# Kernel tuning notes

Measured on AMD Instinct MI355X. Metric: run time of the kernel, lower is better.

## Reference

```python
import jax, jax.numpy as jnp
import numpy as np

B, T, V, H = 1, 1024, 32000, 2048
NH, NKV, HD = 8, 4, 256
QS, KVS = NH * HD, NKV * HD
I, L = 8192, 2
SCALE = 256.0 ** -0.5          # query_pre_attn_scalar ** -0.5
ATTN_CAP, FINAL_CAP = 50.0, 30.0
WIN, EPS, THETA = 512, 1e-6, 10000.0
NEG = -2.3819763e38


def setup_inputs() -> dict:
    key = jax.random.key(0)
    ks = jax.random.split(key, 12)
    s = 0.02
    return {
        "tokens": jax.random.randint(ks[0], (B, T), 0, V, dtype=jnp.int32),
        "embed": jax.random.normal(ks[1], (V, H), jnp.float32) * s,
        "qkv_w": jax.random.normal(ks[2], (L, (NH + 2 * NKV) * HD, H), jnp.float32) * s,
        "o_w": jax.random.normal(ks[3], (L, H, NH * HD), jnp.float32) * s,
        "gate_w": jax.random.normal(ks[4], (L, I, H), jnp.float32) * s,
        "up_w": jax.random.normal(ks[5], (L, I, H), jnp.float32) * s,
        "down_w": jax.random.normal(ks[6], (L, H, I), jnp.float32) * s,
        "ln_in": jax.random.normal(ks[7], (L, H), jnp.float32) * s,   # RMSNorm weight (zeros-init offset)
        "ln_pa": jax.random.normal(ks[8], (L, H), jnp.float32) * s,
        "ln_pre": jax.random.normal(ks[9], (L, H), jnp.float32) * s,
        "ln_post": jax.random.normal(ks[10], (L, H), jnp.float32) * s,
        "ln_f": jax.random.normal(ks[11], (H,), jnp.float32) * s,
    }


def rmsnorm(x, w):
    x = x.astype(jnp.float32)
    n = x * jax.lax.rsqrt(jnp.mean(x * x, axis=-1, keepdims=True) + EPS)
    return n * (1.0 + w)  # add_unit_offset=True


def rope(x, cos, sin):
    # x: [B, T, N, HD]; split-half complex rotary as in apply_rotary_emb
    x1, x2 = jnp.split(x, 2, axis=-1)
    c = cos[None, :, None, :]
    s = sin[None, :, None, :]
    return jnp.concatenate([x1 * c - x2 * s, x1 * s + x2 * c], axis=-1)


def reference(tokens, embed, qkv_w, o_w, gate_w, up_w, down_w,
              ln_in, ln_pa, ln_pre, ln_post, ln_f):
    pos = jnp.arange(T)
    inv = 1.0 / (THETA ** (jnp.arange(0, HD, 2, dtype=jnp.float32) / HD))  # [HD/2]
    ang = pos.astype(jnp.float32)[:, None] * inv[None, :]
    cos, sin = jnp.cos(ang), jnp.sin(ang)

    i, j = pos[:, None], pos[None, :]
    causal = j <= i
    mask_global = jnp.where(causal, 0.0, NEG).astype(jnp.float32)
    mask_local = jnp.where(causal & (i - j < WIN), 0.0, NEG).astype(jnp.float32)
    masks = [mask_local, mask_global]  # layer 0: LOCAL_SLIDING, layer 1: GLOBAL

    x = embed[tokens] * jnp.sqrt(jnp.float32(H))  # Gemma embedding normalizer

    for l in range(L):
        h = rmsnorm(x, ln_in[l])
        qkv = jnp.einsum('bth,oh->bto', h, qkv_w[l])
        q = qkv[..., :QS].reshape(B, T, NH, HD)
        k = qkv[..., QS:QS + KVS].reshape(B, T, NKV, HD)
        v = qkv[..., QS + KVS:].reshape(B, T, NKV, HD)
        q = rope(q, cos, sin)
        k = rope(k, cos, sin)
        # prefill: kv_write_indices=arange(T) -> cache == current k/v
        k = jnp.repeat(k, NH // NKV, axis=2)  # GQA repeat_interleave over heads
        v = jnp.repeat(v, NH // NKV, axis=2)
        scores = jnp.einsum('bqhd,bkhd->bhqk', q * SCALE, k)
        scores = jnp.tanh(scores / ATTN_CAP) * ATTN_CAP
        scores = scores + masks[l][None, None]
        attn = jax.nn.softmax(scores.astype(jnp.float32), axis=-1)
        out = jnp.einsum('bhqk,bkhd->bqhd', attn, v).reshape(B, T, NH * HD)
        out = jnp.einsum('bto,ho->bth', out, o_w[l])
        x = x + rmsnorm(out, ln_pa[l])

        h = rmsnorm(x, ln_pre[l])
        gate = jax.nn.gelu(jnp.einsum('bth,ih->bti', h, gate_w[l]), approximate=True)
        up = jnp.einsum('bth,ih->bti', h, up_w[l])
        ff = jnp.einsum('bti,hi->bth', gate * up, down_w[l])
        x = x + rmsnorm(ff, ln_post[l])

    x = rmsnorm(x, ln_f)
    logits = jnp.einsum('bth,vh->btv', x, embed)
    logits = jnp.tanh(logits / FINAL_CAP) * FINAL_CAP  # final_logit_softcapping
    return logits
```

## Files before the change

### kernel.cpp

```cpp
#include <hip/hip_runtime.h>
#include <hip/hip_bf16.h>
#include <math.h>

typedef unsigned short u16;
typedef __attribute__((ext_vector_type(8))) short bf16x8;
typedef __attribute__((ext_vector_type(4))) float f32x4;
typedef __attribute__((ext_vector_type(4))) u16 u16x4;

#define T_SEQ 1024
#define HDIM  2048
#define NHEAD 8
#define NKVH  4
#define HSZ   256
#define ISZ   8192
#define NVOC  32000

#define GLDS(src, dst) __builtin_amdgcn_global_load_lds( \
    (const __attribute__((address_space(1))) void*)(src), \
    (__attribute__((address_space(3))) void*)(dst), 16, 0, 0)

__device__ __forceinline__ u16 f2bf(float f) {
    union { float f; unsigned u; } v; v.f = f;
    return (u16)((v.u + 0x7fffu + ((v.u >> 16) & 1u)) >> 16);
}
__device__ __forceinline__ float bf2f(u16 h) {
    union { unsigned u; float f; } v; v.u = (unsigned)h << 16; return v.f;
}

__device__ __forceinline__ float fast_tanh(float x) {
    float e = __expf(-2.0f * fabsf(x));
    float t = (1.0f - e) / (1.0f + e);
    return copysignf(t, x);
}

__device__ __forceinline__ f32x4 mfma16(bf16x8 a, bf16x8 b, f32x4 c) {
    return __builtin_amdgcn_mfma_f32_16x16x32_bf16(a, b, c, 0, 0, 0);
}

__global__ __launch_bounds__(256)
void cvt_bf16(const float* __restrict__ s, u16* __restrict__ d, long n4)
{
    for (long i = blockIdx.x * 256L + threadIdx.x; i < n4; i += (long)gridDim.x * 256) {
        f32x4 v = ((const f32x4*)s)[i];
        u16x4 o;
        o.x = f2bf(v.x); o.y = f2bf(v.y); o.z = f2bf(v.z); o.w = f2bf(v.w);
        ((u16x4*)d)[i] = o;
    }
}

template<int EPI>
__global__ __launch_bounds__(512, 1)
void gemm_dp(const u16* __restrict__ A, int lda,
             const u16* __restrict__ B, int ldb,
             float* __restrict__ C, int ldc, long sC, int K)
{
    extern __shared__ u16 lds[];
    const int t = threadIdx.x;
    const int lane = t & 63, wid = t >> 6;
    const int z = blockIdx.z;
    A += (long)z * K;
    B += (long)z * K;
    C += (long)z * sC;

    const int nwg = gridDim.x * gridDim.y;
    int flat = blockIdx.y * gridDim.x + blockIdx.x;
    {
        const int q = nwg >> 3, r = nwg & 7;
        const int xcd = flat & 7, loc = flat >> 3;
        flat = (xcd < r ? xcd * (q + 1) : r * (q + 1) + (xcd - r) * q) + loc;
    }
    const int gm = gridDim.y;
    const long m0 = (long)(flat % gm) * 128;
    const long n0 = (long)(flat / gm) * 256;

    const int sr = t >> 3;
    const int sl = ((t & 7) ^ (sr & 7)) * 8;
    const u16* gA0 = A + (m0 + sr)       * (long)lda + sl;
    const u16* gA1 = A + (m0 + 64 + sr)  * (long)lda + sl;
    const u16* gB0 = B + (n0 + sr)       * (long)ldb + sl;
    const u16* gB1 = B + (n0 + 64 + sr)  * (long)ldb + sl;
    const u16* gB2 = B + (n0 + 128 + sr) * (long)ldb + sl;
    const u16* gB3 = B + (n0 + 192 + sr) * (long)ldb + sl;

    auto stage = [&](int kt) {
        const long ko = (long)kt * 64;
        char* d = (char*)lds + (kt % 3) * 49152 + t * 16;
        GLDS(gA0 + ko, d);
        GLDS(gA1 + ko, d + 8192);
        GLDS(gB0 + ko, d + 16384);
        GLDS(gB1 + ko, d + 24576);
        GLDS(gB2 + ko, d + 32768);
        GLDS(gB3 + ko, d + 40960);
    };

    f32x4 acc[4][4] = {};
    const int fr = lane & 15, kq = lane >> 4;
    const int wm = wid >> 2, wn = wid & 3;
    const int ps0 = ((kq)     ^ (lane & 7)) * 8;
    const int ps1 = ((4 + kq) ^ (lane & 7)) * 8;

    const int KT = K >> 6;
    stage(0);
    if (KT > 1) stage(1);
    if (KT > 2) stage(2);

    for (int kt = 0; kt < KT; ++kt) {
        if (kt < KT - 2)       asm volatile("s_waitcnt vmcnt(12)" ::: "memory");
        else if (kt == KT - 2) asm volatile("s_waitcnt vmcnt(6)" ::: "memory");
        else                   asm volatile("s_waitcnt vmcnt(0)" ::: "memory");
        __builtin_amdgcn_s_barrier();

        const u16* Asl = lds + (kt % 3) * 24576;
        const u16* Bsl = Asl + 8192;
        #pragma unroll
        for (int kk = 0; kk < 2; ++kk) {
            const int ps = kk ? ps1 : ps0;
            bf16x8 af[4], bfv[4];
            #pragma unroll
            for (int mi = 0; mi < 4; ++mi)
                af[mi] = *(const bf16x8*)(Asl + (wm * 64 + mi * 16 + fr) * 64 + ps);
            #pragma unroll
            for (int ni = 0; ni < 4; ++ni)
                bfv[ni] = *(const bf16x8*)(Bsl + (wn * 64 + ni * 16 + fr) * 64 + ps);
            #pragma unroll
            for (int mi = 0; mi < 4; ++mi)
                #pragma unroll
                for (int ni = 0; ni < 4; ++ni)
                    acc[mi][ni] = mfma16(af[mi], bfv[ni], acc[mi][ni]);
        }
        __builtin_amdgcn_s_barrier();
        if (kt + 3 < KT) stage(kt + 3);
    }

    const int crb = kq * 4, ccol = fr;
    #pragma unroll
    for (int mi = 0; mi < 4; ++mi) {
        #pragma unroll
        for (int rr = 0; rr < 4; ++rr) {
            const long row = m0 + wm * 64 + mi * 16 + crb + rr;
            float* cp = C + row * ldc + n0 + wn * 64 + ccol;
            #pragma unroll
            for (int ni = 0; ni < 4; ++ni) {
                float v = acc[mi][ni][rr];
                if (EPI == 1) v = fast_tanh(v * (1.0f / 30.0f)) * 30.0f;
                cp[ni * 16] = v;
            }
        }
    }
}

template<int EPI>
__global__ __launch_bounds__(512, 1)
void gemm8(const u16* __restrict__ A, int lda,
           const u16* __restrict__ B, int ldb,
           float* __restrict__ C, int ldc, long sC, int K)
{
    extern __shared__ u16 lds[];
    const int t = threadIdx.x;
    const int lane = t & 63, wid = t >> 6;
    const int z = blockIdx.z;
    A += (long)z * K;
    B += (long)z * K;
    C += (long)z * sC;

    const int nwg = gridDim.x * gridDim.y;
    int flat = blockIdx.y * gridDim.x + blockIdx.x;
    {
        const int q = nwg >> 3, r = nwg & 7;
        const int xcd = flat & 7, loc = flat >> 3;
        flat = (xcd < r ? xcd * (q + 1) : r * (q + 1) + (xcd - r) * q) + loc;
    }
    const int gm = gridDim.y;
    const long m0 = (long)(flat % gm) * 256;
    const long n0 = (long)(flat / gm) * 256;

    const int sr = t >> 3;
    const int sl = ((t & 7) ^ (sr & 7)) * 8;
    const u16* gA = A + (m0 + sr) * (long)lda + sl;
    const u16* gB = B + (n0 + sr) * (long)ldb + sl;

    auto stA = [&](int kt, int ro) {
        char* d = (char*)lds + (kt & 1) * 65536 + ro * 128 + t * 16;
        GLDS(gA + (long)ro * lda + (long)kt * 64, d);
    };
    auto stB = [&](int kt, int ro) {
        char* d = (char*)lds + (kt & 1) * 65536 + 32768 + ro * 128 + t * 16;
        GLDS(gB + (long)ro * ldb + (long)kt * 64, d);
    };

    f32x4 acc[8][4] = {};
    const int fr = lane & 15, kq = lane >> 4;
    const int wm = wid >> 2, wn = wid & 3;
    const int g0 = ((kq) ^ (lane & 7)) * 8;
    const int g1 = ((4 + kq) ^ (lane & 7)) * 8;
    const int KT = K >> 6;

    stA(0, 0); stA(0, 64); stA(0, 128); stA(0, 192);
    stB(0, 0); stB(0, 64); stB(0, 128); stB(0, 192);
    stA(1, 0); stA(1, 64); stA(1, 128); stA(1, 192);
    stB(1, 0); stB(1, 64); stB(1, 128); stB(1, 192);
    asm volatile("s_waitcnt vmcnt(8)" ::: "memory");
    __builtin_amdgcn_s_barrier();

    for (int kt = 0; kt < KT; ++kt) {
        const u16* As = lds + (kt & 1) * 32768;
        const u16* Bs = As + 16384;
        const int arow = wm * 128 + fr;
        const int brow = wn * 64 + fr;
        bf16x8 aL[4][2], aH[4][2], bL[2][2], bH[2][2];

        #pragma unroll
        for (int mi = 0; mi < 4; ++mi) {
            aL[mi][0] = *(const bf16x8*)(As + (arow + mi * 16) * 64 + g0);
            aL[mi][1] = *(const bf16x8*)(As + (arow + mi * 16) * 64 + g1);
        }
        #pragma unroll
        for (int ni = 0; ni < 2; ++ni) {
            bL[ni][0] = *(const bf16x8*)(Bs + (brow + ni * 16) * 64 + g0);
            bL[ni][1] = *(const bf16x8*)(Bs + (brow + ni * 16) * 64 + g1);
        }
        __builtin_amdgcn_s_setprio(1);
        #pragma unroll
        for (int mi = 0; mi < 4; ++mi)
            #pragma unroll
            for (int ni = 0; ni < 2; ++ni) {
                acc[mi][ni] = mfma16(aL[mi][0], bL[ni][0], acc[mi][ni]);
                acc[mi][ni] = mfma16(aL[mi][1], bL[ni][1], acc[mi][ni]);
            }
        __builtin_amdgcn_s_setprio(0);

        #pragma unroll
        for (int ni = 0; ni < 2; ++ni) {
            bH[ni][0] = *(const bf16x8*)(Bs + (brow + (ni + 2) * 16) * 64 + g0);
            bH[ni][1] = *(const bf16x8*)(Bs + (brow + (ni + 2) * 16) * 64 + g1);
        }
        __builtin_amdgcn_s_setprio(1);
        #pragma unroll
        for (int mi = 0; mi < 4; ++mi)
            #pragma unroll
            for (int ni = 0; ni < 2; ++ni) {
                acc[mi][ni + 2] = mfma16(aL[mi][0], bH[ni][0], acc[mi][ni + 2]);
                acc[mi][ni + 2] = mfma16(aL[mi][1], bH[ni][1], acc[mi][ni + 2]);
            }
        __builtin_amdgcn_s_setprio(0);
        __builtin_amdgcn_s_barrier();

        if (kt + 2 < KT) { stB(kt + 2, 0); stB(kt + 2, 64); stB(kt + 2, 128); stB(kt + 2, 192); }
        #pragma unroll
        for (int mi = 0; mi < 4; ++mi) {
            aH[mi][0] = *(const bf16x8*)(As + (arow + (mi + 4) * 16) * 64 + g0);
            aH[mi][1] = *(const bf16x8*)(As + (arow + (mi + 4) * 16) * 64 + g1);
        }
        __builtin_amdgcn_s_setprio(1);
        #pragma unroll
        for (int mi = 0; mi < 4; ++mi)
            #pragma unroll
            for (int ni = 0; ni < 2; ++ni) {
                acc[mi + 4][ni] = mfma16(aH[mi][0], bL[ni][0], acc[mi + 4][ni]);
                acc[mi + 4][ni] = mfma16(aH[mi][1], bL[ni][1], acc[mi + 4][ni]);
            }
        __builtin_amdgcn_s_setprio(0);
        __builtin_amdgcn_s_barrier();

        if (kt + 2 < KT) { stA(kt + 2, 0); stA(kt + 2, 64); stA(kt + 2, 128); stA(kt + 2, 192); }
        __builtin_amdgcn_s_setprio(1);
        #pragma unroll
        for (int mi = 0; mi < 4; ++mi)
            #pragma unroll
            for (int ni = 0; ni < 2; ++ni) {
                acc[mi + 4][ni + 2] = mfma16(aH[mi][0], bH[ni][0], acc[mi + 4][ni + 2]);
                acc[mi + 4][ni + 2] = mfma16(aH[mi][1], bH[ni][1], acc[mi + 4][ni + 2]);
            }
        __builtin_amdgcn_s_setprio(0);
        if (kt + 1 < KT) {
            if (kt + 2 < KT) asm volatile("s_waitcnt vmcnt(8)" ::: "memory");
            else             asm volatile("s_waitcnt vmcnt(0)" ::: "memory");
            __builtin_amdgcn_s_barrier();
        }
    }

    const int crb = kq * 4, ccol = fr;
    #pragma unroll
    for (int mj = 0; mj < 8; ++mj) {
        #pragma unroll
        for (int rr = 0; rr < 4; ++rr) {
            const long row = m0 + wm * 128 + mj * 16 + crb + rr;
            float* cp = C + row * ldc + n0 + wn * 64 + ccol;
            #pragma unroll
            for (int ni = 0; ni < 4; ++ni) {
                float v = acc[mj][ni][rr];
                if (EPI == 1) v = fast_tanh(v * (1.0f / 30.0f)) * 30.0f;
                cp[ni * 16] = v;
            }
        }
    }
}

template<int EPI, typename CT>
__global__ __launch_bounds__(256)
void gemm_bt(const u16* __restrict__ A, int lda, long sA,
             const u16* __restrict__ B, int ldb, long sB, int bshift,
             CT* __restrict__ C, int ldc, long sC, int K,
             int swin, int tflag)
{
    __shared__ u16 As[128 * 32];
    __shared__ u16 Bs[128 * 32];
    const int tid = threadIdx.x;
    const int lane = tid & 63, wid = tid >> 6;
    const int z = blockIdx.z;
    A += (long)z * sA;
    B += (long)(z >> bshift) * sB;
    C += (long)z * sC;

    const int nwg = gridDim.x * gridDim.y;
    int flat = blockIdx.y * gridDim.x + blockIdx.x;
    {
        const int q = nwg >> 3, r = nwg & 7;
        const int xcd = flat & 7, loc = flat >> 3;
        flat = (xcd < r ? xcd * (q + 1) : r * (q + 1) + (xcd - r) * q) + loc;
    }
    const int gm = gridDim.y;
    const long m0 = (long)(flat % gm) * 128;
    const long n0 = (long)(flat / gm) * 128;

    if (swin > 0) {
        if (n0 > m0 + 127) return;
        if (m0 - (n0 + 127) >= swin) return;
    }
    int klo = 0, khi = K;
    if (tflag > 0) {
        const long hi = m0 + 128;
        if (hi < khi) khi = (int)hi;
        const long lo = m0 - (long)tflag + 1;
        klo = lo > 0 ? (int)(lo & ~31L) : 0;
    }

    f32x4 acc[4][4] = {};

    const int ar = tid >> 2, ac = (tid & 3) * 8;
    const u16* gA0 = A + (m0 + ar) * lda + ac;
    const u16* gB0 = B + (n0 + ar) * (long)ldb + ac;
    const long a64 = 64L * lda, b64 = 64L * ldb;

    const int fr = lane & 15, fk = (lane >> 4) * 8;
    const int wm = (wid >> 1) * 64, wn = (wid & 1) * 64;

    for (int k0 = klo; k0 < khi; k0 += 32) {
        GLDS(gA0 + k0,       &As[tid * 8]);
        GLDS(gA0 + a64 + k0, &As[2048 + tid * 8]);
        GLDS(gB0 + k0,       &Bs[tid * 8]);
        GLDS(gB0 + b64 + k0, &Bs[2048 + tid * 8]);
        __syncthreads();
        bf16x8 af[4], bfv[4];
        #pragma unroll
        for (int mi = 0; mi < 4; ++mi)
            af[mi] = *(const bf16x8*)(&As[(wm + mi * 16 + fr) * 32 + fk]);
        #pragma unroll
        for (int ni = 0; ni < 4; ++ni)
            bfv[ni] = *(const bf16x8*)(&Bs[(wn + ni * 16 + fr) * 32 + fk]);
        #pragma unroll
        for (int mi = 0; mi < 4; ++mi)
            #pragma unroll
            for (int ni = 0; ni < 4; ++ni)
                acc[mi][ni] = mfma16(af[mi], bfv[ni], acc[mi][ni]);
        __syncthreads();
    }

    const int crb = (lane >> 4) * 4, ccol = lane & 15;
    #pragma unroll
    for (int mi = 0; mi < 4; ++mi) {
        #pragma unroll
        for (int rr = 0; rr < 4; ++rr) {
            const long row = m0 + wm + mi * 16 + crb + rr;
            CT* cp = C + row * ldc + n0 + wn + ccol;
            #pragma unroll
            for (int ni = 0; ni < 4; ++ni) {
                float v = acc[mi][ni][rr];
                if (EPI == 1) v = fast_tanh(v * (1.0f / 30.0f)) * 30.0f;
                if constexpr (sizeof(CT) == 2) cp[ni * 16] = f2bf(v);
                else                           cp[ni * 16] = v;
            }
        }
    }
}

__global__ __launch_bounds__(256)
void embed_scale(const int* __restrict__ tok, const float* __restrict__ emb,
                 float* __restrict__ x)
{
    const int t = blockIdx.x, tid = threadIdx.x;
    const long src = (long)tok[t] * HDIM;
    f32x4 a = *(const f32x4*)(emb + src + tid * 8);
    f32x4 b = *(const f32x4*)(emb + src + tid * 8 + 4);
    a *= 45.254834f; b *= 45.254834f;
    *(f32x4*)(x + (long)t * HDIM + tid * 8) = a;
    *(f32x4*)(x + (long)t * HDIM + tid * 8 + 4) = b;
}

__device__ __forceinline__ float block_sum(float v, float* red) {
    #pragma unroll
    for (int o = 32; o; o >>= 1) v += __shfl_xor(v, o);
    const int tid = threadIdx.x;
    if ((tid & 63) == 0) red[tid >> 6] = v;
    __syncthreads();
    return red[0] + red[1] + red[2] + red[3];
}

__global__ __launch_bounds__(256)
void rmsnorm_bf16(const float* __restrict__ x, const float* __restrict__ w,
                  u16* __restrict__ out)
{
    __shared__ float red[4];
    const int t = blockIdx.x, tid = threadIdx.x;
    const float* row = x + (long)t * HDIM;
    f32x4 a = *(const f32x4*)(row + tid * 8);
    f32x4 b = *(const f32x4*)(row + tid * 8 + 4);
    float ss = a.x*a.x + a.y*a.y + a.z*a.z + a.w*a.w
             + b.x*b.x + b.y*b.y + b.z*b.z + b.w*b.w;
    ss = block_sum(ss, red);
    const float r = rsqrtf(ss * (1.0f / HDIM) + 1e-6f);
    f32x4 wa = *(const f32x4*)(w + tid * 8);
    f32x4 wb = *(const f32x4*)(w + tid * 8 + 4);
    u16x4 o0, o1;
    o0.x = f2bf(a.x * r * (1.0f + wa.x)); o0.y = f2bf(a.y * r * (1.0f + wa.y));
    o0.z = f2bf(a.z * r * (1.0f + wa.z)); o0.w = f2bf(a.w * r * (1.0f + wa.w));
    o1.x = f2bf(b.x * r * (1.0f + wb.x)); o1.y = f2bf(b.y * r * (1.0f + wb.y));
    o1.z = f2bf(b.z * r * (1.0f + wb.z)); o1.w = f2bf(b.w * r * (1.0f + wb.w));
    *(u16x4*)(out + (long)t * HDIM + tid * 8) = o0;
    *(u16x4*)(out + (long)t * HDIM + tid * 8 + 4) = o1;
}

__global__ __launch_bounds__(256)
void add_rmsnorm(float* __restrict__ x, const float* __restrict__ y,
                 const float* __restrict__ w, int nsplit, long stride)
{
    __shared__ float red[4];
    const int t = blockIdx.x, tid = threadIdx.x;
    const float* yr = y + (long)t * HDIM;
    f32x4 a = *(const f32x4*)(yr + tid * 8);
    f32x4 b = *(const f32x4*)(yr + tid * 8 + 4);
    for (int s = 1; s < nsplit; ++s) {
        a += *(const f32x4*)(yr + s * stride + tid * 8);
        b += *(const f32x4*)(yr + s * stride + tid * 8 + 4);
    }
    float ss = a.x*a.x + a.y*a.y + a.z*a.z + a.w*a.w
             + b.x*b.x + b.y*b.y + b.z*b.z + b.w*b.w;
    ss = block_sum(ss, red);
    const float r = rsqrtf(ss * (1.0f / HDIM) + 1e-6f);
    f32x4 wa = *(const f32x4*)(w + tid * 8);
    f32x4 wb = *(const f32x4*)(w + tid * 8 + 4);
    float* xr = x + (long)t * HDIM;
    f32x4 xa = *(const f32x4*)(xr + tid * 8);
    f32x4 xb = *(const f32x4*)(xr + tid * 8 + 4);
    xa.x += a.x * r * (1.0f + wa.x); xa.y += a.y * r * (1.0f + wa.y);
    xa.z += a.z * r * (1.0f + wa.z); xa.w += a.w * r * (1.0f + wa.w);
    xb.x += b.x * r * (1.0f + wb.x); xb.y += b.y * r * (1.0f + wb.y);
    xb.z += b.z * r * (1.0f + wb.z); xb.w += b.w * r * (1.0f + wb.w);
    *(f32x4*)(xr + tid * 8) = xa;
    *(f32x4*)(xr + tid * 8 + 4) = xb;
}

#define QKV_STRIDE (1024L * 4096)

__global__ __launch_bounds__(256)
void qkv_post(const float* __restrict__ qkv, u16* __restrict__ qb,
              u16* __restrict__ kb)
{
    const int t = blockIdx.x, tid = threadIdx.x;
    const float* row = qkv + (long)t * 4096;
    const float ft = (float)t;
    #pragma unroll
    for (int it = 0; it < 4; ++it) {
        const int p = tid + it * 256;
        const int nh = p >> 7, d = p & 127;
        const float inv = powf(10000.0f, -(float)d * (1.0f / 128.0f));
        const float ang = ft * inv;
        const float c = cosf(ang), s = sinf(ang);
        const int i1 = nh * 256 + d, i2 = i1 + 128;
        const float x1 = row[i1] + row[i1 + QKV_STRIDE];
        const float x2 = row[i2] + row[i2 + QKV_STRIDE];
        const long ob = ((long)nh * T_SEQ + t) * HSZ;
        qb[ob + d]       = f2bf((x1 * c - x2 * s) * 0.0625f);
        qb[ob + 128 + d] = f2bf((x1 * s + x2 * c) * 0.0625f);
    }
    #pragma unroll
    for (int it = 0; it < 2; ++it) {
        const int p = tid + it * 256;
        const int kv = p >> 7, d = p & 127;
        const float inv = powf(10000.0f, -(float)d * (1.0f / 128.0f));
        const float ang = ft * inv;
        const float c = cosf(ang), s = sinf(ang);
        const int i1 = 2048 + kv * 256 + d, i2 = i1 + 128;
        const float x1 = row[i1] + row[i1 + QKV_STRIDE];
        const float x2 = row[i2] + row[i2 + QKV_STRIDE];
        const long ob = ((long)kv * T_SEQ + t) * HSZ;
        kb[ob + d]       = f2bf(x1 * c - x2 * s);
        kb[ob + 128 + d] = f2bf(x1 * s + x2 * c);
    }
}

__global__ __launch_bounds__(256)
void v_transpose(const float* __restrict__ qkvb, u16* __restrict__ vT)
{
    __shared__ u16 tile[64][65];
    const int t0 = blockIdx.x * 64, d0 = blockIdx.y * 64, kv = blockIdx.z;
    const int lane = threadIdx.x & 63, w = threadIdx.x >> 6;
    #pragma unroll
    for (int i = 0; i < 16; ++i) {
        const int t = w * 16 + i;
        const long idx = (long)(t0 + t) * 4096 + 3072 + kv * 256 + d0 + lane;
        tile[t][lane] = f2bf(qkvb[idx] + qkvb[idx + QKV_STRIDE]);
    }
    __syncthreads();
    #pragma unroll
    for (int i = 0; i < 16; ++i) {
        const int d = w * 16 + i;
        vT[((long)kv * HSZ + d0 + d) * T_SEQ + t0 + lane] = tile[lane][d];
    }
}

__global__ __launch_bounds__(256)
void softmax_mask(const float* __restrict__ sc, u16* __restrict__ pr, int win)
{
    __shared__ float redm[4], reds[4];
    const int i = blockIdx.x, h = blockIdx.y, tid = threadIdx.x;
    const long base = ((long)h * T_SEQ + i) * T_SEQ;
    f32x4 sv = *(const f32x4*)(sc + base + tid * 4);
    float vals[4];
    #pragma unroll
    for (int j = 0; j < 4; ++j) {
        const int col = tid * 4 + j;
        const float s = fast_tanh(sv[j] * 0.02f) * 50.0f;
        const bool valid = (col <= i) && ((i - col) < win);
        vals[j] = valid ? s : -3.0e38f;
    }
    float m = fmaxf(fmaxf(vals[0], vals[1]), fmaxf(vals[2], vals[3]));
    #pragma unroll
    for (int o = 32; o; o >>= 1) m = fmaxf(m, __shfl_xor(m, o));
    if ((tid & 63) == 0) redm[tid >> 6] = m;
    __syncthreads();
    m = fmaxf(fmaxf(redm[0], redm[1]), fmaxf(redm[2], redm[3]));
    float sum = 0.0f;
    #pragma unroll
    for (int j = 0; j < 4; ++j) { vals[j] = __expf(vals[j] - m); sum += vals[j]; }
    #pragma unroll
    for (int o = 32; o; o >>= 1) sum += __shfl_xor(sum, o);
    if ((tid & 63) == 0) reds[tid >> 6] = sum;
    __syncthreads();
    sum = reds[0] + reds[1] + reds[2] + reds[3];
    const float inv = 1.0f / sum;
    u16x4 o4;
    #pragma unroll
    for (int j = 0; j < 4; ++j) o4[j] = f2bf(vals[j] * inv);
    *(u16x4*)(pr + base + tid * 4) = o4;
}

__global__ __launch_bounds__(256)
void mul_gelu(const float* __restrict__ g, const float* __restrict__ u,
              u16* __restrict__ p)
{
    const int n4 = (T_SEQ * ISZ) / 4;
    for (int i = blockIdx.x * 256 + threadIdx.x; i < n4; i += gridDim.x * 256) {
        f32x4 gv = ((const f32x4*)g)[i];
        f32x4 uv = ((const f32x4*)u)[i];
        u16x4 w;
        #pragma unroll
        for (int j = 0; j < 4; ++j) {
            const float xg = gv[j];
            const float tt = fast_tanh(0.79788456f * (xg + 0.044715f * xg * xg * xg));
            w[j] = f2bf(0.5f * xg * (1.0f + tt) * uv[j]);
        }
        ((u16x4*)p)[i] = w;
    }
}

extern "C" void kernel_launch(void* const* d_in, const int* in_sizes, int n_in,
                              void* d_out, int out_size, void* d_ws, size_t ws_size,
                              hipStream_t stream)
{
    (void)in_sizes; (void)n_in; (void)out_size; (void)ws_size;
    const int*   tokens = (const int*)  d_in[0];
    const float* emb    = (const float*)d_in[1];
    const float* qkv_w  = (const float*)d_in[2];
    const float* o_w    = (const float*)d_in[3];
    const float* gate_w = (const float*)d_in[4];
    const float* up_w   = (const float*)d_in[5];
    const float* down_w = (const float*)d_in[6];
    const float* ln_in  = (const float*)d_in[7];
    const float* ln_pa  = (const float*)d_in[8];
    const float* ln_pre = (const float*)d_in[9];
    const float* ln_post= (const float*)d_in[10];
    const float* ln_f   = (const float*)d_in[11];
    float* logits = (float*)d_out;

    char* base = (char*)d_ws;
    size_t off = 0;
    auto alloc = [&](size_t b) { char* p = base + off; off += (b + 255) & ~(size_t)255; return p; };

    float* x    = (float*)alloc((size_t)T_SEQ * HDIM * 4);
    u16*   hb   = (u16*)  alloc((size_t)T_SEQ * HDIM * 2);
    u16*   qb   = (u16*)  alloc((size_t)NHEAD * T_SEQ * HSZ * 2);
    u16*   kb   = (u16*)  alloc((size_t)NKVH * T_SEQ * HSZ * 2);
    u16*   vT   = (u16*)  alloc((size_t)NKVH * HSZ * T_SEQ * 2);
    u16*   ao   = (u16*)  alloc((size_t)T_SEQ * HDIM * 2);
    u16*   pb   = (u16*)  alloc((size_t)T_SEQ * ISZ * 2);
    char*  big  = alloc((size_t)2 * T_SEQ * ISZ * 4);
    float* P    = (float*)big;
    float* sc   = (float*)big;
    u16*   pr   = (u16*)(big + (size_t)NHEAD * T_SEQ * T_SEQ * 4);
    float* gb   = (float*)big;
    float* ub   = (float*)(big + (size_t)T_SEQ * ISZ * 4);
    u16*   wb   = (u16*)  alloc((size_t)NVOC * HDIM * 2);

    const size_t LDSD = 3 * 49152;
    const size_t LDS8 = 2 * 65536;
    const long s2048 = 1024L * 2048;
    const int BIGWIN = 1 << 29;

    embed_scale<<<T_SEQ, 256, 0, stream>>>(tokens, emb, x);
    for (int l = 0; l < 2; ++l) {
        const int win = (l == 0) ? 512 : BIGWIN;
        rmsnorm_bf16<<<T_SEQ, 256, 0, stream>>>(x, ln_in + l * HDIM, hb);
        cvt_bf16<<<2048, 256, 0, stream>>>(qkv_w + (size_t)l * 4096 * HDIM, wb, 4096L * HDIM / 4);
        gemm_dp<0><<<dim3(16, 8, 2), 512, LDSD, stream>>>(
            hb, HDIM, wb, HDIM, P, 4096, QKV_STRIDE, 1024);
        qkv_post<<<T_SEQ, 256, 0, stream>>>(P, qb, kb);
        v_transpose<<<dim3(16, 4, 4), 256, 0, stream>>>(P, vT);
        gemm_bt<0, float><<<dim3(8, 8, NHEAD), 256, 0, stream>>>(
            qb, HSZ, (long)T_SEQ * HSZ, kb, HSZ, (long)T_SEQ * HSZ, 1,
            sc, T_SEQ, (long)T_SEQ * T_SEQ, HSZ, win, 0);
        softmax_mask<<<dim3(T_SEQ, NHEAD, 1), 256, 0, stream>>>(
            sc, pr, l == 0 ? 512 : (1 << 30));
        gemm_bt<0, u16><<<dim3(2, 8, NHEAD), 256, 0, stream>>>(
            pr, T_SEQ, (long)T_SEQ * T_SEQ, vT, T_SEQ, (long)HSZ * T_SEQ, 1,
            ao, HDIM, (long)HSZ, T_SEQ, 0, win);
        cvt_bf16<<<2048, 256, 0, stream>>>(o_w + (size_t)l * HDIM * HDIM, wb, (long)HDIM * HDIM / 4);
        gemm_dp<0><<<dim3(8, 8, 4), 512, LDSD, stream>>>(
            ao, HDIM, wb, HDIM, P, HDIM, s2048, 512);
        add_rmsnorm<<<T_SEQ, 256, 0, stream>>>(x, P, ln_pa + l * HDIM, 4, s2048);
        rmsnorm_bf16<<<T_SEQ, 256, 0, stream>>>(x, ln_pre + l * HDIM, hb);
        cvt_bf16<<<2048, 256, 0, stream>>>(gate_w + (size_t)l * ISZ * HDIM, wb, (long)ISZ * HDIM / 4);
        gemm_dp<0><<<dim3(32, 8, 1), 512, LDSD, stream>>>(
            hb, HDIM, wb, HDIM, gb, ISZ, 0, HDIM);
        cvt_bf16<<<2048, 256, 0, stream>>>(up_w + (size_t)l * ISZ * HDIM, wb, (long)ISZ * HDIM / 4);
        gemm_dp<0><<<dim3(32, 8, 1), 512, LDSD, stream>>>(
            hb, HDIM, wb, HDIM, ub, ISZ, 0, HDIM);
        mul_gelu<<<2048, 256, 0, stream>>>(gb, ub, pb);
        cvt_bf16<<<2048, 256, 0, stream>>>(down_w + (size_t)l * HDIM * ISZ, wb, (long)HDIM * ISZ / 4);
        gemm_dp<0><<<dim3(8, 8, 4), 512, LDSD, stream>>>(
            pb, ISZ, wb, ISZ, P, HDIM, s2048, 2048);
        add_rmsnorm<<<T_SEQ, 256, 0, stream>>>(x, P, ln_post + l * HDIM, 4, s2048);
    }
    rmsnorm_bf16<<<T_SEQ, 256, 0, stream>>>(x, ln_f, hb);
    cvt_bf16<<<2048, 256, 0, stream>>>(emb, wb, (long)NVOC * HDIM / 4);
    gemm8<1><<<dim3(125, 4, 1), 512, LDS8, stream>>>(
        hb, HDIM, wb, HDIM, logits, NVOC, 0, HDIM);
}
```

Before: 875.6 us.

## Shrink GEMM K-tile and staging to raise occupancy with MFMA priority hints

The split-K/direct GEMM kernel now stages 32-wide K slices in a double buffer (48 KB LDS) instead of 64-wide slices in a triple buffer (144 KB). Launch bounds are raised to allow up to 4 workgroups per CU. The LDS swizzle is redone for 4 chunks per row, and s_setprio is wrapped around the MFMA block. The aim is to hide latency through more resident workgroups rather than a deeper prefetch, at the cost of more barriers per unit of K, less prefetch depth, and register pressure under the tighter launch bound.

```diff
diff --git a/kernel.cpp b/kernel.cpp
--- a/kernel.cpp
+++ b/kernel.cpp
@@ -49,10 +49,10 @@
 }
 
 template<int EPI>
-__global__ __launch_bounds__(512, 1)
-void gemm_dp(const u16* __restrict__ A, int lda,
-             const u16* __restrict__ B, int ldb,
-             float* __restrict__ C, int ldc, long sC, int K)
+__global__ __launch_bounds__(512, 4)
+void gemm_l(const u16* __restrict__ A, int lda,
+            const u16* __restrict__ B, int ldb,
+            float* __restrict__ C, int ldc, long sC, int K)
 {
     extern __shared__ u16 lds[];
     const int t = threadIdx.x;
@@ -73,63 +73,54 @@
     const long m0 = (long)(flat % gm) * 128;
     const long n0 = (long)(flat / gm) * 256;
 
-    const int sr = t >> 3;
-    const int sl = ((t & 7) ^ (sr & 7)) * 8;
-    const u16* gA0 = A + (m0 + sr)       * (long)lda + sl;
-    const u16* gA1 = A + (m0 + 64 + sr)  * (long)lda + sl;
-    const u16* gB0 = B + (n0 + sr)       * (long)ldb + sl;
-    const u16* gB1 = B + (n0 + 64 + sr)  * (long)ldb + sl;
-    const u16* gB2 = B + (n0 + 128 + sr) * (long)ldb + sl;
-    const u16* gB3 = B + (n0 + 192 + sr) * (long)ldb + sl;
+    const int srow = t >> 2;
+    const int skey = (srow ^ (srow >> 2)) & 3;
+    const int sl = ((t & 3) ^ skey) * 8;
+    const u16* gA0 = A + (m0 + srow)       * (long)lda + sl;
+    const u16* gB0 = B + (n0 + srow)       * (long)ldb + sl;
+    const u16* gB1 = B + (n0 + 128 + srow) * (long)ldb + sl;
 
     auto stage = [&](int kt) {
-        const long ko = (long)kt * 64;
-        char* d = (char*)lds + (kt % 3) * 49152 + t * 16;
+        const long ko = (long)kt * 32;
+        char* d = (char*)lds + (kt & 1) * 24576 + t * 16;
         GLDS(gA0 + ko, d);
-        GLDS(gA1 + ko, d + 8192);
-        GLDS(gB0 + ko, d + 16384);
-        GLDS(gB1 + ko, d + 24576);
-        GLDS(gB2 + ko, d + 32768);
-        GLDS(gB3 + ko, d + 40960);
+        GLDS(gB0 + ko, d + 8192);
+        GLDS(gB1 + ko, d + 16384);
     };
 
     f32x4 acc[4][4] = {};
     const int fr = lane & 15, kq = lane >> 4;
     const int wm = wid >> 2, wn = wid & 3;
-    const int ps0 = ((kq)     ^ (lane & 7)) * 8;
-    const int ps1 = ((4 + kq) ^ (lane & 7)) * 8;
-
-    const int KT = K >> 6;
+    const int rkey = (fr ^ (fr >> 2)) & 3;
+    const int g = ((kq ^ rkey) & 3) * 8;
+
+    const int KT = K >> 5;
     stage(0);
-    if (KT > 1) stage(1);
-    if (KT > 2) stage(2);
+    stage(1);
 
     for (int kt = 0; kt < KT; ++kt) {
-        if (kt < KT - 2)       asm volatile("s_waitcnt vmcnt(12)" ::: "memory");
-        else if (kt == KT - 2) asm volatile("s_waitcnt vmcnt(6)" ::: "memory");
-        else                   asm volatile("s_waitcnt vmcnt(0)" ::: "memory");
+        if (kt < KT - 1) asm volatile("s_waitcnt vmcnt(3)" ::: "memory");
+        else             asm volatile("s_waitcnt vmcnt(0)" ::: "memory");
         __builtin_amdgcn_s_barrier();
 
-        const u16* Asl = lds + (kt % 3) * 24576;
-        const u16* Bsl = Asl + 8192;
-        #pragma unroll
-        for (int kk = 0; kk < 2; ++kk) {
-            const int ps = kk ? ps1 : ps0;
-            bf16x8 af[4], bfv[4];
-            #pragma unroll
-            for (int mi = 0; mi < 4; ++mi)
-                af[mi] = *(const bf16x8*)(Asl + (wm * 64 + mi * 16 + fr) * 64 + ps);
+        const u16* Asl = lds + (kt & 1) * 12288;
+        const u16* Bsl = Asl + 4096;
+        bf16x8 af[4], bfv[4];
+        #pragma unroll
+        for (int mi = 0; mi < 4; ++mi)
+            af[mi] = *(const bf16x8*)(Asl + (wm * 64 + mi * 16 + fr) * 32 + g);
+        #pragma unroll
+        for (int ni = 0; ni < 4; ++ni)
+            bfv[ni] = *(const bf16x8*)(Bsl + (wn * 64 + ni * 16 + fr) * 32 + g);
+        __builtin_amdgcn_s_setprio(1);
+        #pragma unroll
+        for (int mi = 0; mi < 4; ++mi)
             #pragma unroll
             for (int ni = 0; ni < 4; ++ni)
-                bfv[ni] = *(const bf16x8*)(Bsl + (wn * 64 + ni * 16 + fr) * 64 + ps);
-            #pragma unroll
-            for (int mi = 0; mi < 4; ++mi)
-                #pragma unroll
-                for (int ni = 0; ni < 4; ++ni)
-                    acc[mi][ni] = mfma16(af[mi], bfv[ni], acc[mi][ni]);
-        }
+                acc[mi][ni] = mfma16(af[mi], bfv[ni], acc[mi][ni]);
+        __builtin_amdgcn_s_setprio(0);
         __builtin_amdgcn_s_barrier();
-        if (kt + 3 < KT) stage(kt + 3);
+        if (kt + 2 < KT) stage(kt + 2);
     }
 
     const int crb = kq * 4, ccol = fr;
@@ -612,7 +603,7 @@
     float* ub   = (float*)(big + (size_t)T_SEQ * ISZ * 4);
     u16*   wb   = (u16*)  alloc((size_t)NVOC * HDIM * 2);
 
-    const size_t LDSD = 3 * 49152;
+    const size_t LDSL = 2 * 24576;
     const size_t LDS8 = 2 * 65536;
     const long s2048 = 1024L * 2048;
     const int BIGWIN = 1 << 29;
@@ -622,7 +613,7 @@
         const int win = (l == 0) ? 512 : BIGWIN;
         rmsnorm_bf16<<<T_SEQ, 256, 0, stream>>>(x, ln_in + l * HDIM, hb);
         cvt_bf16<<<2048, 256, 0, stream>>>(qkv_w + (size_t)l * 4096 * HDIM, wb, 4096L * HDIM / 4);
-        gemm_dp<0><<<dim3(16, 8, 2), 512, LDSD, stream>>>(
+        gemm_l<0><<<dim3(16, 8, 2), 512, LDSL, stream>>>(
             hb, HDIM, wb, HDIM, P, 4096, QKV_STRIDE, 1024);
         qkv_post<<<T_SEQ, 256, 0, stream>>>(P, qb, kb);
         v_transpose<<<dim3(16, 4, 4), 256, 0, stream>>>(P, vT);
@@ -635,19 +626,19 @@
             pr, T_SEQ, (long)T_SEQ * T_SEQ, vT, T_SEQ, (long)HSZ * T_SEQ, 1,
             ao, HDIM, (long)HSZ, T_SEQ, 0, win);
         cvt_bf16<<<2048, 256, 0, stream>>>(o_w + (size_t)l * HDIM * HDIM, wb, (long)HDIM * HDIM / 4);
-        gemm_dp<0><<<dim3(8, 8, 4), 512, LDSD, stream>>>(
+        gemm_l<0><<<dim3(8, 8, 4), 512, LDSL, stream>>>(
             ao, HDIM, wb, HDIM, P, HDIM, s2048, 512);
         add_rmsnorm<<<T_SEQ, 256, 0, stream>>>(x, P, ln_pa + l * HDIM, 4, s2048);
         rmsnorm_bf16<<<T_SEQ, 256, 0, stream>>>(x, ln_pre + l * HDIM, hb);
         cvt_bf16<<<2048, 256, 0, stream>>>(gate_w + (size_t)l * ISZ * HDIM, wb, (long)ISZ * HDIM / 4);
-        gemm_dp<0><<<dim3(32, 8, 1), 512, LDSD, stream>>>(
+        gemm_l<0><<<dim3(32, 8, 1), 512, LDSL, stream>>>(
             hb, HDIM, wb, HDIM, gb, ISZ, 0, HDIM);
         cvt_bf16<<<2048, 256, 0, stream>>>(up_w + (size_t)l * ISZ * HDIM, wb, (long)ISZ * HDIM / 4);
-        gemm_dp<0><<<dim3(32, 8, 1), 512, LDSD, stream>>>(
+        gemm_l<0><<<dim3(32, 8, 1), 512, LDSL, stream>>>(
             hb, HDIM, wb, HDIM, ub, ISZ, 0, HDIM);
         mul_gelu<<<2048, 256, 0, stream>>>(gb, ub, pb);
         cvt_bf16<<<2048, 256, 0, stream>>>(down_w + (size_t)l * HDIM * ISZ, wb, (long)HDIM * ISZ / 4);
-        gemm_dp<0><<<dim3(8, 8, 4), 512, LDSD, stream>>>(
+        gemm_l<0><<<dim3(8, 8, 4), 512, LDSL, stream>>>(
             pb, ISZ, wb, ISZ, P, HDIM, s2048, 2048);
         add_rmsnorm<<<T_SEQ, 256, 0, stream>>>(x, P, ln_post + l * HDIM, 4, s2048);
     }
```

Measured after the change: 911.3 us. +4.1%, slower.
